# Optimization experiments

Measured on AMD Instinct MI355X. Metric: run time of the kernel, lower is better.

## Reference

```python
import jax, jax.numpy as jnp
import numpy as np

N, E, F_IN, G = 100000, 1600000, 128, 64
H1, H2, H3 = 64, 32, 16


def _xavier(key, fan_in, fan_out):
    lim = np.sqrt(6.0 / (fan_in + fan_out))
    return jax.random.uniform(key, (fan_in, fan_out), jnp.float32, -lim, lim)


def setup_inputs() -> dict:
    key = jax.random.key(0)
    ks = jax.random.split(key, 16)
    x = jax.random.normal(ks[0], (N, F_IN), jnp.float32)
    edge_index = jax.random.randint(ks[1], (2, E), 0, N, dtype=jnp.int32)
    batch = jnp.sort(jax.random.randint(ks[2], (N,), 0, G, dtype=jnp.int32))
    d = {
        "x": x,
        "W1": _xavier(ks[3], F_IN, H1), "b1": jnp.zeros((H1,), jnp.float32),
        "W2": _xavier(ks[4], H1, H2), "b2": jnp.zeros((H2,), jnp.float32),
        "W3": _xavier(ks[5], H2, H3), "b3": jnp.zeros((H3,), jnp.float32),
        "g1": jnp.ones((H1,), jnp.float32), "be1": jnp.zeros((H1,), jnp.float32),
        "g2": jnp.ones((H2,), jnp.float32), "be2": jnp.zeros((H2,), jnp.float32),
        "g3": jnp.ones((H3,), jnp.float32), "be3": jnp.zeros((H3,), jnp.float32),
        "attn_w": _xavier(ks[6], 3 * H3, 3), "attn_b": jnp.zeros((3,), jnp.float32),
        "fc1_w": _xavier(ks[7], H3, H3), "fc1_b": jnp.zeros((H3,), jnp.float32),
        "fc2_w": _xavier(ks[8], H3, H3 // 2), "fc2_b": jnp.zeros((H3 // 2,), jnp.float32),
        "out_w": _xavier(ks[9], H3 // 2, 1), "out_b": jnp.zeros((1,), jnp.float32),
        "edge_index": edge_index,
        "batch": batch,
        "num_graphs": G,
    }
    return d


def _lrelu(z):
    return jnp.where(z > 0, z, 0.1 * z)


def _bn(h, gamma, beta, eps=1e-5):
    # BatchNorm1d forward with batch statistics (biased variance), as torch training-mode math
    m = jnp.mean(h, axis=0)
    v = jnp.mean(jnp.square(h - m), axis=0)
    return (h - m) * jax.lax.rsqrt(v + eps) * gamma + beta


def reference(x, W1, b1, W2, b2, W3, b3, g1, be1, g2, be2, g3, be3,
              attn_w, attn_b, fc1_w, fc1_b, fc2_w, fc2_b, out_w, out_b,
              edge_index, batch, num_graphs):
    src, dst = edge_index[0], edge_index[1]
    n = x.shape[0]
    # GCN degree with self-loops: deg[i] = 1 + #incoming edges
    deg = jax.ops.segment_sum(jnp.ones((src.shape[0],), x.dtype), dst, num_segments=n) + 1.0
    dis = jax.lax.rsqrt(deg)                      # deg^-1/2, [N]
    enorm = dis[src] * dis[dst]                   # per-edge norm, [E]
    selfw = dis * dis                             # self-loop norm, [N]

    def gcn(h, W, b):
        hw = h @ W                                # [N, H]
        agg = jax.ops.segment_sum(hw[src] * enorm[:, None], dst, num_segments=n)
        return agg + selfw[:, None] * hw + b

    x1 = _lrelu(_bn(gcn(x, W1, b1), g1, be1))     # dropout = identity (eval)
    x2 = _lrelu(_bn(gcn(x1, W2, b2), g2, be2))    # residual skipped: 64 != 32
    x3 = _lrelu(_bn(gcn(x2, W3, b3), g3, be3))    # residual skipped: 32 != 16

    # multi-pool over graphs
    ones_n = jnp.ones((n,), x.dtype)
    counts = jax.ops.segment_sum(ones_n, batch, num_segments=num_graphs)  # [G]
    x_sum = jax.ops.segment_sum(x3, batch, num_segments=num_graphs)       # [G, H3]
    x_mean = x_sum / jnp.maximum(counts, 1.0)[:, None]
    x_max = jax.ops.segment_max(x3, batch, num_segments=num_graphs)

    pooled = jnp.concatenate([x_mean, x_max, x_sum], axis=1)              # [G, 3*H3]
    aw = jax.nn.softmax(pooled @ attn_w + attn_b, axis=1)                 # [G, 3]
    xg = aw[:, 0:1] * x_mean + aw[:, 1:2] * x_max + aw[:, 2:3] * x_sum    # [G, H3]

    xg = _lrelu(xg @ fc1_w + fc1_b)
    xg = _lrelu(xg @ fc2_w + fc2_b)
    out = jax.nn.sigmoid(xg @ out_w + out_b)                              # [G, 1]
    return out
```

## Files before the change

kernel.cpp:

```cpp
#include <hip/hip_runtime.h>

#define GG 64
typedef unsigned long long ull;
typedef unsigned short u16;

__device__ __forceinline__ u16 f2b(float x) {
    unsigned u = __float_as_uint(x);
    return (u16)((u + 0x7FFFu + ((u >> 16) & 1u)) >> 16);
}

__device__ __forceinline__ void fma8(const uint4 q, float w, float* acc) {
    acc[0] = fmaf(__uint_as_float(q.x << 16), w, acc[0]);
    acc[1] = fmaf(__uint_as_float(q.x & 0xFFFF0000u), w, acc[1]);
    acc[2] = fmaf(__uint_as_float(q.y << 16), w, acc[2]);
    acc[3] = fmaf(__uint_as_float(q.y & 0xFFFF0000u), w, acc[3]);
    acc[4] = fmaf(__uint_as_float(q.z << 16), w, acc[4]);
    acc[5] = fmaf(__uint_as_float(q.z & 0xFFFF0000u), w, acc[5]);
    acc[6] = fmaf(__uint_as_float(q.w << 16), w, acc[6]);
    acc[7] = fmaf(__uint_as_float(q.w & 0xFFFF0000u), w, acc[7]);
}

__global__ void k_hist(const int* __restrict__ dst, int* __restrict__ cnt, int E) {
    int e = blockIdx.x * blockDim.x + threadIdx.x;
    if (e < E) atomicAdd(&cnt[dst[e]], 1);
}

__global__ void k_dis(const int* __restrict__ cnt, float* __restrict__ dis, int n) {
    int i = blockIdx.x * blockDim.x + threadIdx.x;
    if (i < n) dis[i] = rsqrtf((float)cnt[i] + 1.0f);
}

__global__ void k_scanA(const int* __restrict__ cnt, int* __restrict__ rp,
                        int* __restrict__ bsum, int n) {
    __shared__ int s[256];
    int i = blockIdx.x * 256 + threadIdx.x;
    int v = (i < n) ? cnt[i] : 0;
    s[threadIdx.x] = v;
    __syncthreads();
    for (int off = 1; off < 256; off <<= 1) {
        int t = (threadIdx.x >= off) ? s[threadIdx.x - off] : 0;
        __syncthreads();
        s[threadIdx.x] += t;
        __syncthreads();
    }
    if (i < n) rp[i] = s[threadIdx.x] - v;
    if (threadIdx.x == 255) bsum[blockIdx.x] = s[255];
}

__global__ void k_scanB(int* __restrict__ bsum, int nb) {
    __shared__ int s[512];
    int v = (threadIdx.x < nb) ? bsum[threadIdx.x] : 0;
    s[threadIdx.x] = v;
    __syncthreads();
    for (int off = 1; off < 512; off <<= 1) {
        int t = (threadIdx.x >= off) ? s[threadIdx.x - off] : 0;
        __syncthreads();
        s[threadIdx.x] += t;
        __syncthreads();
    }
    if (threadIdx.x < nb) bsum[threadIdx.x] = s[threadIdx.x] - v;
}

__global__ void k_scanC(int* __restrict__ rp, const int* __restrict__ bsum,
                        int* __restrict__ cursor, int n, int E) {
    int i = blockIdx.x * 256 + threadIdx.x;
    if (i < n) {
        int r = rp[i] + bsum[blockIdx.x];
        rp[i] = r;
        cursor[i] = r;
    }
    if (i == 0) rp[n] = E;
}

__global__ void k_scatter(const int* __restrict__ src, const int* __restrict__ dst,
                          const float* __restrict__ dis, int* __restrict__ cursor,
                          ull* __restrict__ epack, int E) {
    int e = blockIdx.x * blockDim.x + threadIdx.x;
    if (e >= E) return;
    int s = src[e], d = dst[e];
    float w = dis[s] * dis[d];
    int pos = atomicAdd(&cursor[d], 1);
    epack[pos] = ((ull)__float_as_uint(w) << 32) | (unsigned)s;
}

template <int FIN, int FOUT>
__global__ __launch_bounds__(256) void k_mm(const float* __restrict__ h,
                                            const float* __restrict__ W,
                                            u16* __restrict__ hw, int n) {
    constexpr int FX  = FOUT / 4;
    constexpr int TY  = 256 / FX;
    constexpr int NT  = TY * 4;
    constexpr int LDA = FIN + ((FOUT == 64) ? 2 : 1);
    __shared__ float sA[NT * LDA];
    __shared__ float sW[FIN * FOUT];

    for (int i = threadIdx.x; i < FIN * FOUT / 4; i += 256)
        ((float4*)sW)[i] = ((const float4*)W)[i];

    const int node0 = blockIdx.x * NT;
    constexpr int LD4 = NT * FIN / 4 / 256;
    #pragma unroll
    for (int i = 0; i < LD4; ++i) {
        int idx4 = i * 256 + threadIdx.x;
        int row = idx4 / (FIN / 4);
        int c4  = idx4 % (FIN / 4);
        int gn  = node0 + row;
        float4 v = make_float4(0.f, 0.f, 0.f, 0.f);
        if (gn < n) v = ((const float4*)(h + (long long)gn * FIN))[c4];
        float* p = &sA[row * LDA + c4 * 4];
        p[0] = v.x; p[1] = v.y; p[2] = v.z; p[3] = v.w;
    }
    __syncthreads();

    const int tx = threadIdx.x % FX;
    const int ty = threadIdx.x / FX;
    float acc[4][4];
    #pragma unroll
    for (int i = 0; i < 4; ++i)
        #pragma unroll
        for (int j = 0; j < 4; ++j) acc[i][j] = 0.f;

    #pragma unroll 8
    for (int k = 0; k < FIN; ++k) {
        float4 wv = *((const float4*)&sW[k * FOUT + tx * 4]);
        float a0 = sA[(ty * 4 + 0) * LDA + k];
        float a1 = sA[(ty * 4 + 1) * LDA + k];
        float a2 = sA[(ty * 4 + 2) * LDA + k];
        float a3 = sA[(ty * 4 + 3) * LDA + k];
        acc[0][0] = fmaf(a0, wv.x, acc[0][0]); acc[0][1] = fmaf(a0, wv.y, acc[0][1]);
        acc[0][2] = fmaf(a0, wv.z, acc[0][2]); acc[0][3] = fmaf(a0, wv.w, acc[0][3]);
        acc[1][0] = fmaf(a1, wv.x, acc[1][0]); acc[1][1] = fmaf(a1, wv.y, acc[1][1]);
        acc[1][2] = fmaf(a1, wv.z, acc[1][2]); acc[1][3] = fmaf(a1, wv.w, acc[1][3]);
        acc[2][0] = fmaf(a2, wv.x, acc[2][0]); acc[2][1] = fmaf(a2, wv.y, acc[2][1]);
        acc[2][2] = fmaf(a2, wv.z, acc[2][2]); acc[2][3] = fmaf(a2, wv.w, acc[2][3]);
        acc[3][0] = fmaf(a3, wv.x, acc[3][0]); acc[3][1] = fmaf(a3, wv.y, acc[3][1]);
        acc[3][2] = fmaf(a3, wv.z, acc[3][2]); acc[3][3] = fmaf(a3, wv.w, acc[3][3]);
    }

    #pragma unroll
    for (int i = 0; i < 4; ++i) {
        int gn = node0 + ty * 4 + i;
        if (gn < n) {
            ushort4 o;
            o.x = f2b(acc[i][0]); o.y = f2b(acc[i][1]);
            o.z = f2b(acc[i][2]); o.w = f2b(acc[i][3]);
            ((ushort4*)(hw + (long long)gn * FOUT))[tx] = o;
        }
    }
}

template <int FOUT>
__global__ __launch_bounds__(256) void k_agg(const u16* __restrict__ hwb,
                                             const ull* __restrict__ epack,
                                             const int* __restrict__ rp,
                                             const float* __restrict__ dis,
                                             const float* __restrict__ bias,
                                             float* __restrict__ y,
                                             float* __restrict__ stats, int n) {
    constexpr int LPN = FOUT / 8;
    constexpr int NPB = 256 / LPN;
    constexpr int RS  = FOUT / 8;
    __shared__ float ssum[FOUT], ssq[FOUT];
    for (int i = threadIdx.x; i < FOUT; i += 256) { ssum[i] = 0.f; ssq[i] = 0.f; }
    __syncthreads();
    const int local = threadIdx.x / LPN;
    const int fq = threadIdx.x % LPN;
    const uint4* hw4 = (const uint4*)hwb;
    float b8[8];
    #pragma unroll
    for (int i = 0; i < 8; ++i) b8[i] = bias[fq * 8 + i];
    float lsum[8] = {0,0,0,0,0,0,0,0}, lsq[8] = {0,0,0,0,0,0,0,0};

    for (long long base = (long long)blockIdx.x * NPB; base < n;
         base += (long long)gridDim.x * NPB) {
        int node = (int)base + local;
        if (node >= n) continue;
        int j0 = rp[node], j1 = rp[node + 1];
        float acc[8] = {0,0,0,0,0,0,0,0};
        int j = j0;
        for (; j + 4 <= j1; j += 4) {
            ull p0 = epack[j + 0], p1 = epack[j + 1];
            ull p2 = epack[j + 2], p3 = epack[j + 3];
            uint4 q0 = hw4[(long long)(unsigned)p0 * RS + fq];
            uint4 q1 = hw4[(long long)(unsigned)p1 * RS + fq];
            uint4 q2 = hw4[(long long)(unsigned)p2 * RS + fq];
            uint4 q3 = hw4[(long long)(unsigned)p3 * RS + fq];
            fma8(q0, __uint_as_float((unsigned)(p0 >> 32)), acc);
            fma8(q1, __uint_as_float((unsigned)(p1 >> 32)), acc);
            fma8(q2, __uint_as_float((unsigned)(p2 >> 32)), acc);
            fma8(q3, __uint_as_float((unsigned)(p3 >> 32)), acc);
        }
        for (; j < j1; ++j) {
            ull p = epack[j];
            uint4 q = hw4[(long long)(unsigned)p * RS + fq];
            fma8(q, __uint_as_float((unsigned)(p >> 32)), acc);
        }
        float dv = dis[node];
        float sw = dv * dv;
        uint4 qs = hw4[(long long)node * RS + fq];
        fma8(qs, sw, acc);
        #pragma unroll
        for (int i = 0; i < 8; ++i) acc[i] += b8[i];
        float4* y4 = (float4*)y;
        long long o = (long long)node * (FOUT / 4) + fq * 2;
        y4[o]     = make_float4(acc[0], acc[1], acc[2], acc[3]);
        y4[o + 1] = make_float4(acc[4], acc[5], acc[6], acc[7]);
        #pragma unroll
        for (int i = 0; i < 8; ++i) {
            lsum[i] += acc[i];
            lsq[i] = fmaf(acc[i], acc[i], lsq[i]);
        }
    }
    #pragma unroll
    for (int i = 0; i < 8; ++i) {
        atomicAdd(&ssum[fq * 8 + i], lsum[i]);
        atomicAdd(&ssq[fq * 8 + i], lsq[i]);
    }
    __syncthreads();
    for (int i = threadIdx.x; i < FOUT; i += 256) {
        atomicAdd(&stats[i], ssum[i]);
        atomicAdd(&stats[64 + i], ssq[i]);
    }
}

__global__ void k_bn(float* __restrict__ y, const float* __restrict__ stats,
                     const float* __restrict__ gma, const float* __restrict__ bta,
                     int n, int fout_shift) {
    long long tid = (long long)blockIdx.x * blockDim.x + threadIdx.x;
    if (tid >= ((long long)n << fout_shift)) return;
    int f = (int)(tid & ((1 << fout_shift) - 1));
    float inv_n = 1.0f / (float)n;
    float m = stats[f] * inv_n;
    float var = fmaxf(stats[64 + f] * inv_n - m * m, 0.f);
    float sc = rsqrtf(var + 1e-5f) * gma[f];
    float sh = bta[f] - m * sc;
    float v = y[tid] * sc + sh;
    y[tid] = v > 0.f ? v : 0.1f * v;
}

__global__ void k_pool_graph(const float* __restrict__ h, const int* __restrict__ batch,
                             int n, float* __restrict__ psum, float* __restrict__ pmax,
                             float* __restrict__ pcnt) {
    const int g = blockIdx.x;
    __shared__ int s_lo, s_hi;
    if (threadIdx.x == 0) {
        int lo = 0, hi = n;
        while (lo < hi) { int mid = (lo + hi) >> 1; if (batch[mid] < g) lo = mid + 1; else hi = mid; }
        s_lo = lo;
        hi = n;
        while (lo < hi) { int mid = (lo + hi) >> 1; if (batch[mid] < g + 1) lo = mid + 1; else hi = mid; }
        s_hi = lo;
    }
    __syncthreads();
    const int start = s_lo, end = s_hi;
    float lsum = 0.f, lmax = -3.0e38f;
    for (long long idx = (long long)start * 16 + threadIdx.x; idx < (long long)end * 16; idx += blockDim.x) {
        float v = h[idx];
        lsum += v;
        lmax = fmaxf(lmax, v);
    }
    __shared__ float ss[256], sm[256];
    ss[threadIdx.x] = lsum; sm[threadIdx.x] = lmax;
    __syncthreads();
    for (int off = 128; off >= 16; off >>= 1) {
        if (threadIdx.x < off) {
            ss[threadIdx.x] += ss[threadIdx.x + off];
            sm[threadIdx.x] = fmaxf(sm[threadIdx.x], sm[threadIdx.x + off]);
        }
        __syncthreads();
    }
    if (threadIdx.x < 16) {
        psum[g * 16 + threadIdx.x] = ss[threadIdx.x];
        pmax[g * 16 + threadIdx.x] = sm[threadIdx.x];
    }
    if (threadIdx.x == 0) pcnt[g] = (float)(end - start);
}

__global__ void k_head(const float* __restrict__ psum, const float* __restrict__ pmax,
                       const float* __restrict__ pcnt,
                       const float* __restrict__ attn_w, const float* __restrict__ attn_b,
                       const float* __restrict__ fc1_w, const float* __restrict__ fc1_b,
                       const float* __restrict__ fc2_w, const float* __restrict__ fc2_b,
                       const float* __restrict__ out_w, const float* __restrict__ out_b,
                       float* __restrict__ out) {
    int g = threadIdx.x;
    if (g >= GG) return;
    float xs[16], xm[16], xx[16];
    float c = fmaxf(pcnt[g], 1.0f);
    for (int f = 0; f < 16; ++f) {
        xs[f] = psum[(g << 4) + f];
        xm[f] = xs[f] / c;
        xx[f] = pmax[(g << 4) + f];
    }
    float lg[3];
    for (int cI = 0; cI < 3; ++cI) {
        float a = attn_b[cI];
        for (int f = 0; f < 16; ++f) {
            a += xm[f] * attn_w[f * 3 + cI];
            a += xx[f] * attn_w[(16 + f) * 3 + cI];
            a += xs[f] * attn_w[(32 + f) * 3 + cI];
        }
        lg[cI] = a;
    }
    float mx = fmaxf(lg[0], fmaxf(lg[1], lg[2]));
    float e0 = expf(lg[0] - mx), e1 = expf(lg[1] - mx), e2 = expf(lg[2] - mx);
    float inv = 1.0f / (e0 + e1 + e2);
    float a0 = e0 * inv, a1 = e1 * inv, a2 = e2 * inv;
    float xg[16];
    for (int f = 0; f < 16; ++f) xg[f] = a0 * xm[f] + a1 * xx[f] + a2 * xs[f];
    float t1[16];
    for (int j = 0; j < 16; ++j) {
        float a = fc1_b[j];
        for (int k = 0; k < 16; ++k) a += xg[k] * fc1_w[k * 16 + j];
        t1[j] = a > 0.f ? a : 0.1f * a;
    }
    float t2[8];
    for (int j = 0; j < 8; ++j) {
        float a = fc2_b[j];
        for (int k = 0; k < 16; ++k) a += t1[k] * fc2_w[k * 8 + j];
        t2[j] = a > 0.f ? a : 0.1f * a;
    }
    float o = out_b[0];
    for (int k = 0; k < 8; ++k) o += t2[k] * out_w[k];
    o = 1.0f / (1.0f + expf(-o));
    out[g] = o;
}

extern "C" void kernel_launch(void* const* d_in, const int* in_sizes, int n_in,
                              void* d_out, int out_size, void* d_ws, size_t ws_size,
                              hipStream_t stream) {
    const float* x      = (const float*)d_in[0];
    const float* W1     = (const float*)d_in[1];  const float* b1   = (const float*)d_in[2];
    const float* W2     = (const float*)d_in[3];  const float* b2   = (const float*)d_in[4];
    const float* W3     = (const float*)d_in[5];  const float* b3   = (const float*)d_in[6];
    const float* g1     = (const float*)d_in[7];  const float* be1  = (const float*)d_in[8];
    const float* g2     = (const float*)d_in[9];  const float* be2  = (const float*)d_in[10];
    const float* g3     = (const float*)d_in[11]; const float* be3  = (const float*)d_in[12];
    const float* attn_w = (const float*)d_in[13]; const float* attn_b = (const float*)d_in[14];
    const float* fc1_w  = (const float*)d_in[15]; const float* fc1_b  = (const float*)d_in[16];
    const float* fc2_w  = (const float*)d_in[17]; const float* fc2_b  = (const float*)d_in[18];
    const float* out_w  = (const float*)d_in[19]; const float* out_b  = (const float*)d_in[20];
    const int* edge_index = (const int*)d_in[21];
    const int* batch      = (const int*)d_in[22];

    const int N = in_sizes[0] / 128;
    const int E = in_sizes[21] / 2;
    const int* srcp = edge_index;
    const int* dstp = edge_index + E;
    const int nb = (N + 255) / 256;

    char* ws = (char*)d_ws;
    float* dis    = (float*)(ws);
    int*   cnt    = (int*)(ws + 0x80000);
    int*   rp     = (int*)(ws + 0x100000);
    int*   bsum   = (int*)(ws + 0x180000);
    float* stats  = (float*)(ws + 0x182000);
    float* psum   = stats + 128;
    float* pmax   = psum + GG * 16;
    float* pcnt   = pmax + GG * 16;
    ull*   epack  = (ull*)(ws + 0x190000);
    float* buf1   = (float*)(ws + 0x190000 + (size_t)E * 8);
    u16*   hwb    = (u16*)(buf1 + (size_t)N * 64);

    hipMemsetAsync(cnt, 0, (size_t)N * 4, stream);
    k_hist<<<(E + 255) / 256, 256, 0, stream>>>(dstp, cnt, E);
    k_dis<<<nb, 256, 0, stream>>>(cnt, dis, N);
    k_scanA<<<nb, 256, 0, stream>>>(cnt, rp, bsum, N);
    k_scanB<<<1, 512, 0, stream>>>(bsum, nb);
    k_scanC<<<nb, 256, 0, stream>>>(rp, bsum, cnt, N, E);
    k_scatter<<<(E + 255) / 256, 256, 0, stream>>>(srcp, dstp, dis, cnt, epack, E);

    k_mm<128, 64><<<(N + 63) / 64, 256, 0, stream>>>(x, W1, hwb, N);
    hipMemsetAsync(stats, 0, 512, stream);
    k_agg<64><<<2048, 256, 0, stream>>>(hwb, epack, rp, dis, b1, buf1, stats, N);
    k_bn<<<(unsigned)(((long long)N * 64 + 255) / 256), 256, 0, stream>>>(
        buf1, stats, g1, be1, N, 6);

    k_mm<64, 32><<<(N + 127) / 128, 256, 0, stream>>>(buf1, W2, hwb, N);
    hipMemsetAsync(stats, 0, 512, stream);
    k_agg<32><<<2048, 256, 0, stream>>>(hwb, epack, rp, dis, b2, buf1, stats, N);
    k_bn<<<(unsigned)(((long long)N * 32 + 255) / 256), 256, 0, stream>>>(
        buf1, stats, g2, be2, N, 5);

    k_mm<32, 16><<<(N + 255) / 256, 256, 0, stream>>>(buf1, W3, hwb, N);
    hipMemsetAsync(stats, 0, 512, stream);
    k_agg<16><<<2048, 256, 0, stream>>>(hwb, epack, rp, dis, b3, buf1, stats, N);
    k_bn<<<(unsigned)(((long long)N * 16 + 255) / 256), 256, 0, stream>>>(
        buf1, stats, g3, be3, N, 4);

    k_pool_graph<<<GG, 256, 0, stream>>>(buf1, batch, N, psum, pmax, pcnt);
    k_head<<<1, 64, 0, stream>>>(psum, pmax, pcnt, attn_w, attn_b,
                                 fc1_w, fc1_b, fc2_w, fc2_b, out_w, out_b,
                                 (float*)d_out);
}
```

Measured before the change: 627.5 us.

## Factor symmetric GCN normalization into pre-scaled features and shrink edge list to int32

The source-side deg^-1/2 factor is now applied to the transformed features in the matmul epilogue, and the destination-side factor is applied once per node after aggregation. The per-edge weight therefore disappears, so the CSR edge array holds only 4-byte source indices instead of 8-byte packed weight/index pairs. This halves edge-list traffic in each of the three aggregation passes and removes the dis gathers from the scatter kernel. Aggregation grids are also sized to cover all nodes in a single pass instead of using a fixed 2048 blocks. The price is an extra rounding step, since the features are scaled before bf16 conversion.

```diff
diff --git a/kernel.cpp b/kernel.cpp
--- a/kernel.cpp
+++ b/kernel.cpp
@@ -9,15 +9,15 @@
     return (u16)((u + 0x7FFFu + ((u >> 16) & 1u)) >> 16);
 }
 
-__device__ __forceinline__ void fma8(const uint4 q, float w, float* acc) {
-    acc[0] = fmaf(__uint_as_float(q.x << 16), w, acc[0]);
-    acc[1] = fmaf(__uint_as_float(q.x & 0xFFFF0000u), w, acc[1]);
-    acc[2] = fmaf(__uint_as_float(q.y << 16), w, acc[2]);
-    acc[3] = fmaf(__uint_as_float(q.y & 0xFFFF0000u), w, acc[3]);
-    acc[4] = fmaf(__uint_as_float(q.z << 16), w, acc[4]);
-    acc[5] = fmaf(__uint_as_float(q.z & 0xFFFF0000u), w, acc[5]);
-    acc[6] = fmaf(__uint_as_float(q.w << 16), w, acc[6]);
-    acc[7] = fmaf(__uint_as_float(q.w & 0xFFFF0000u), w, acc[7]);
+__device__ __forceinline__ void add8(const uint4 q, float* acc) {
+    acc[0] += __uint_as_float(q.x << 16);
+    acc[1] += __uint_as_float(q.x & 0xFFFF0000u);
+    acc[2] += __uint_as_float(q.y << 16);
+    acc[3] += __uint_as_float(q.y & 0xFFFF0000u);
+    acc[4] += __uint_as_float(q.z << 16);
+    acc[5] += __uint_as_float(q.z & 0xFFFF0000u);
+    acc[6] += __uint_as_float(q.w << 16);
+    acc[7] += __uint_as_float(q.w & 0xFFFF0000u);
 }
 
 __global__ void k_hist(const int* __restrict__ dst, int* __restrict__ cnt, int E) {
@@ -73,19 +73,18 @@
 }
 
 __global__ void k_scatter(const int* __restrict__ src, const int* __restrict__ dst,
-                          const float* __restrict__ dis, int* __restrict__ cursor,
-                          ull* __restrict__ epack, int E) {
+                          int* __restrict__ cursor, int* __restrict__ epack, int E) {
     int e = blockIdx.x * blockDim.x + threadIdx.x;
     if (e >= E) return;
     int s = src[e], d = dst[e];
-    float w = dis[s] * dis[d];
     int pos = atomicAdd(&cursor[d], 1);
-    epack[pos] = ((ull)__float_as_uint(w) << 32) | (unsigned)s;
+    epack[pos] = s;
 }
 
 template <int FIN, int FOUT>
 __global__ __launch_bounds__(256) void k_mm(const float* __restrict__ h,
                                             const float* __restrict__ W,
+                                            const float* __restrict__ dis,
                                             u16* __restrict__ hw, int n) {
     constexpr int FX  = FOUT / 4;
     constexpr int TY  = 256 / FX;
@@ -141,9 +140,10 @@
     for (int i = 0; i < 4; ++i) {
         int gn = node0 + ty * 4 + i;
         if (gn < n) {
+            float dv = dis[gn];
             ushort4 o;
-            o.x = f2b(acc[i][0]); o.y = f2b(acc[i][1]);
-            o.z = f2b(acc[i][2]); o.w = f2b(acc[i][3]);
+            o.x = f2b(acc[i][0] * dv); o.y = f2b(acc[i][1] * dv);
+            o.z = f2b(acc[i][2] * dv); o.w = f2b(acc[i][3] * dv);
             ((ushort4*)(hw + (long long)gn * FOUT))[tx] = o;
         }
     }
@@ -151,7 +151,7 @@
 
 template <int FOUT>
 __global__ __launch_bounds__(256) void k_agg(const u16* __restrict__ hwb,
-                                             const ull* __restrict__ epack,
+                                             const int* __restrict__ epack,
                                              const int* __restrict__ rp,
                                              const float* __restrict__ dis,
                                              const float* __restrict__ bias,
@@ -179,28 +179,23 @@
         float acc[8] = {0,0,0,0,0,0,0,0};
         int j = j0;
         for (; j + 4 <= j1; j += 4) {
-            ull p0 = epack[j + 0], p1 = epack[j + 1];
-            ull p2 = epack[j + 2], p3 = epack[j + 3];
-            uint4 q0 = hw4[(long long)(unsigned)p0 * RS + fq];
-            uint4 q1 = hw4[(long long)(unsigned)p1 * RS + fq];
-            uint4 q2 = hw4[(long long)(unsigned)p2 * RS + fq];
-            uint4 q3 = hw4[(long long)(unsigned)p3 * RS + fq];
-            fma8(q0, __uint_as_float((unsigned)(p0 >> 32)), acc);
-            fma8(q1, __uint_as_float((unsigned)(p1 >> 32)), acc);
-            fma8(q2, __uint_as_float((unsigned)(p2 >> 32)), acc);
-            fma8(q3, __uint_as_float((unsigned)(p3 >> 32)), acc);
+            int s0 = epack[j + 0], s1 = epack[j + 1];
+            int s2 = epack[j + 2], s3 = epack[j + 3];
+            uint4 q0 = hw4[(long long)s0 * RS + fq];
+            uint4 q1 = hw4[(long long)s1 * RS + fq];
+            uint4 q2 = hw4[(long long)s2 * RS + fq];
+            uint4 q3 = hw4[(long long)s3 * RS + fq];
+            add8(q0, acc); add8(q1, acc); add8(q2, acc); add8(q3, acc);
         }
         for (; j < j1; ++j) {
-            ull p = epack[j];
-            uint4 q = hw4[(long long)(unsigned)p * RS + fq];
-            fma8(q, __uint_as_float((unsigned)(p >> 32)), acc);
-        }
+            uint4 q = hw4[(long long)epack[j] * RS + fq];
+            add8(q, acc);
+        }
+        uint4 qs = hw4[(long long)node * RS + fq];
+        add8(qs, acc);
         float dv = dis[node];
-        float sw = dv * dv;
-        uint4 qs = hw4[(long long)node * RS + fq];
-        fma8(qs, sw, acc);
         #pragma unroll
-        for (int i = 0; i < 8; ++i) acc[i] += b8[i];
+        for (int i = 0; i < 8; ++i) acc[i] = fmaf(dv, acc[i], b8[i]);
         float4* y4 = (float4*)y;
         long long o = (long long)node * (FOUT / 4) + fq * 2;
         y4[o]     = make_float4(acc[0], acc[1], acc[2], acc[3]);
@@ -358,8 +353,8 @@
     float* psum   = stats + 128;
     float* pmax   = psum + GG * 16;
     float* pcnt   = pmax + GG * 16;
-    ull*   epack  = (ull*)(ws + 0x190000);
-    float* buf1   = (float*)(ws + 0x190000 + (size_t)E * 8);
+    int*   epack  = (int*)(ws + 0x190000);
+    float* buf1   = (float*)(ws + 0x190000 + (size_t)E * 4);
     u16*   hwb    = (u16*)(buf1 + (size_t)N * 64);
 
     hipMemsetAsync(cnt, 0, (size_t)N * 4, stream);
@@ -368,23 +363,27 @@
     k_scanA<<<nb, 256, 0, stream>>>(cnt, rp, bsum, N);
     k_scanB<<<1, 512, 0, stream>>>(bsum, nb);
     k_scanC<<<nb, 256, 0, stream>>>(rp, bsum, cnt, N, E);
-    k_scatter<<<(E + 255) / 256, 256, 0, stream>>>(srcp, dstp, dis, cnt, epack, E);
-
-    k_mm<128, 64><<<(N + 63) / 64, 256, 0, stream>>>(x, W1, hwb, N);
+    k_scatter<<<(E + 255) / 256, 256, 0, stream>>>(srcp, dstp, cnt, epack, E);
+
+    const int gr1 = (N + 31) / 32;
+    const int gr2 = (N + 63) / 64;
+    const int gr3 = (N + 127) / 128;
+
+    k_mm<128, 64><<<(N + 63) / 64, 256, 0, stream>>>(x, W1, dis, hwb, N);
     hipMemsetAsync(stats, 0, 512, stream);
-    k_agg<64><<<2048, 256, 0, stream>>>(hwb, epack, rp, dis, b1, buf1, stats, N);
+    k_agg<64><<<gr1, 256, 0, stream>>>(hwb, epack, rp, dis, b1, buf1, stats, N);
     k_bn<<<(unsigned)(((long long)N * 64 + 255) / 256), 256, 0, stream>>>(
         buf1, stats, g1, be1, N, 6);
 
-    k_mm<64, 32><<<(N + 127) / 128, 256, 0, stream>>>(buf1, W2, hwb, N);
+    k_mm<64, 32><<<(N + 127) / 128, 256, 0, stream>>>(buf1, W2, dis, hwb, N);
     hipMemsetAsync(stats, 0, 512, stream);
-    k_agg<32><<<2048, 256, 0, stream>>>(hwb, epack, rp, dis, b2, buf1, stats, N);
+    k_agg<32><<<gr2, 256, 0, stream>>>(hwb, epack, rp, dis, b2, buf1, stats, N);
     k_bn<<<(unsigned)(((long long)N * 32 + 255) / 256), 256, 0, stream>>>(
         buf1, stats, g2, be2, N, 5);
 
-    k_mm<32, 16><<<(N + 255) / 256, 256, 0, stream>>>(buf1, W3, hwb, N);
+    k_mm<32, 16><<<(N + 255) / 256, 256, 0, stream>>>(buf1, W3, dis, hwb, N);
     hipMemsetAsync(stats, 0, 512, stream);
-    k_agg<16><<<2048, 256, 0, stream>>>(hwb, epack, rp, dis, b3, buf1, stats, N);
+    k_agg<16><<<gr3, 256, 0, stream>>>(hwb, epack, rp, dis, b3, buf1, stats, N);
     k_bn<<<(unsigned)(((long long)N * 16 + 255) / 256), 256, 0, stream>>>(
         buf1, stats, g3, be3, N, 4);
 
```

Result: slower. 692.0 us (+10.3%).
